# Kernel optimization log

Measured on AMD Instinct MI355X. Metric: run time of the kernel, lower is better.

## Reference

```python
import jax, jax.numpy as jnp
import numpy as np

# --- static config (mirrors init_kwargs) ---
T = 256          # number of tokens (decode steps)
A = 8            # analyses per token
N = 1 + T * A    # lattice rows (row 0 = start/gold row, token_idx 0)
H = 256          # encoder hidden size (bidirectional -> 2H context)
DH = 2 * H       # decoder hidden size (hidden_size * 2 per AnalysisDecoder)
FV, LV, TV, FEV = 100000, 50000, 100, 500   # vocab sizes
FD, LD, TD, FED = 300, 300, 100, 100        # embedding dims
D = FD + LD + TD + FED                      # 800 = LSTM input size
NEG = -1e10


def setup_inputs() -> dict:
    key = jax.random.key(0)
    ks = jax.random.split(key, 16)
    # structured lattice: [form, lemma, tag, feats x6, token_idx, is_gold]
    rng = np.random.default_rng(0)
    lat = np.zeros((N, 11), np.int64)
    lat[:, 0] = rng.integers(0, FV, N)
    lat[:, 1] = rng.integers(0, LV, N)
    lat[:, 2] = rng.integers(0, TV, N)
    lat[:, 3:9] = rng.integers(0, FEV, (N, 6))
    lat[:, 9] = np.concatenate([[0], np.repeat(np.arange(1, T + 1), A)])  # token_idx
    is_gold = np.zeros(N, np.int64)
    is_gold[0] = 1
    is_gold[1 + np.arange(T) * A] = 1   # exactly one gold analysis per token
    lat[:, 10] = is_gold

    s = 0.05
    def p(k, shape):
        return jax.random.normal(k, shape, dtype=jnp.float32) * s

    return dict(
        lattice=jnp.asarray(lat),
        num_tokens=T,
        form_emb=p(ks[0], (FV, FD)),
        lemma_emb=p(ks[1], (LV, LD)),
        tag_emb=p(ks[2], (TV, TD)),
        feats_emb=p(ks[3], (FEV, FED)),
        enc_wih_f=p(ks[4], (4 * H, D)), enc_whh_f=p(ks[5], (4 * H, H)), enc_b_f=p(ks[6], (4 * H,)),
        enc_wih_b=p(ks[7], (4 * H, D)), enc_whh_b=p(ks[8], (4 * H, H)), enc_b_b=p(ks[9], (4 * H,)),
        dec_wih=p(ks[10], (4 * DH, D)), dec_whh=p(ks[11], (4 * DH, DH)), dec_b=p(ks[12], (4 * DH,)),
    )


def _lstm_scan(xs, Wih, Whh, b, hdim):
    # batch-1 LSTM over a sequence; PyTorch gate order i, f, g, o
    def step(carry, x):
        h, c = carry
        g = Wih @ x + Whh @ h + b
        i, f, gg, o = jnp.split(g, 4)
        c = jax.nn.sigmoid(f) * c + jax.nn.sigmoid(i) * jnp.tanh(gg)
        h = jax.nn.sigmoid(o) * jnp.tanh(c)
        return (h, c), h
    z = jnp.zeros((hdim,), xs.dtype)
    (hT, cT), hs = jax.lax.scan(step, (z, z), xs)
    return hs, hT, cT


def reference(lattice, num_tokens, form_emb, lemma_emb, tag_emb, feats_emb,
              enc_wih_f, enc_whh_f, enc_b_f, enc_wih_b, enc_whh_b, enc_b_b,
              dec_wih, dec_whh, dec_b):
    tok = lattice[:, 9]
    gold = jnp.nonzero(lattice[:, 10], size=num_tokens + 1)[0]  # one gold per token (incl. start)

    # MorphEmbedding: concat of form/lemma/tag embeddings + mean of 6 feat embeddings
    emb = jnp.concatenate([
        form_emb[lattice[:, 0]],
        lemma_emb[lattice[:, 1]],
        tag_emb[lattice[:, 2]],
        feats_emb[lattice[:, 3:9]].mean(axis=1),
    ], axis=1)  # [N, D]

    # bidirectional encoder (dropouts are identity in eval)
    hs_f, hTf, cTf = _lstm_scan(emb, enc_wih_f, enc_whh_f, enc_b_f, H)
    hs_b, hTb, cTb = _lstm_scan(emb[::-1], enc_wih_b, enc_whh_b, enc_b_b, H)
    encoded = jnp.concatenate([hs_f, hs_b[::-1]], axis=1)  # [N, 2H]
    h0 = jnp.concatenate([hTf, hTb])  # decoder init hidden [DH]
    c0 = jnp.concatenate([cTf, cTb])

    # decode loop: NOTE the original never propagates the decoder hidden state
    # across steps (forward() discards the updated state) -- faithfully preserved.
    def dec(x, i):
        g = dec_wih @ x + dec_whh @ h0 + dec_b
        ii, ff, gg, oo = jnp.split(g, 4)
        c = jax.nn.sigmoid(ff) * c0 + jax.nn.sigmoid(ii) * jnp.tanh(gg)
        h = jax.nn.sigmoid(oo) * jnp.tanh(c)
        scores = encoded @ h                       # [N]
        scores = jnp.where(tok == i, scores, NEG)  # masked_fill(mask==0, -1e10)
        logp = jax.nn.log_softmax(scores)          # log_softmax over dim 0
        ptr = jnp.argmax(logp)
        return emb[ptr], (logp, ptr)               # greedy pointer feeds next step

    _, (pred_score, ptrs) = jax.lax.scan(dec, emb[0], jnp.arange(1, num_tokens + 1))
    pred_indices = jnp.concatenate([gold[:1], ptrs])

    # CrossEntropyLoss applied to log-probs (faithful: log_softmax applied again)
    lp = jax.nn.log_softmax(pred_score, axis=1)
    loss = -jnp.mean(lp[jnp.arange(num_tokens), gold[1:]])
    return pred_indices, loss
```

## Files before the change

kernel.cpp:

```cpp
#include <hip/hip_runtime.h>
#include <hip/hip_fp16.h>

#define T_TOK 256
#define NNODE 2049
#define HENC  256
#define DHID  512
#define DIN   800
#define G4    1024
#define DG4   2048

typedef _Float16 f16;
typedef _Float16 f16x2 __attribute__((ext_vector_type(2)));
typedef short    bf16x8 __attribute__((ext_vector_type(8)));
typedef float    f32x4  __attribute__((ext_vector_type(4)));

static __device__ __forceinline__ float sigm(float x){ return 1.0f/(1.0f+__expf(-x)); }
static __device__ __forceinline__ float tanhfast(float x){ return 1.0f - 2.0f/(__expf(2.0f*x)+1.0f); }

static __device__ __forceinline__ unsigned short f2bf(float x){
    unsigned u = __builtin_bit_cast(unsigned, x);
    unsigned r = (u + 0x7fffu + ((u>>16)&1u)) >> 16;
    return (unsigned short)r;
}
static __device__ __forceinline__ unsigned packh2(float a, float b){
    f16 ha = (f16)a, hb = (f16)b;
    unsigned short ua = __builtin_bit_cast(unsigned short, ha);
    unsigned short ub = __builtin_bit_cast(unsigned short, hb);
    return (unsigned)ua | ((unsigned)ub << 16);
}
static __device__ __forceinline__ float fdot2(unsigned wpk, unsigned hpk, float c){
#if __has_builtin(__builtin_amdgcn_fdot2)
    return __builtin_amdgcn_fdot2(__builtin_bit_cast(f16x2, wpk),
                                  __builtin_bit_cast(f16x2, hpk), c, false);
#else
    float d;
    asm volatile("v_dot2_f32_f16 %0, %1, %2, %3" : "=v"(d) : "v"(wpk), "v"(hpk), "v"(c));
    return d;
#endif
}

static __device__ __forceinline__ uint4 ldw_opaque(const uint4* p){
    uint4 r;
    asm volatile("global_load_dwordx4 %0, %1, off\n\ts_waitcnt vmcnt(0)"
                 : "=v"(r) : "v"(p));
    return r;
}

__global__ void k_embed(const int* __restrict__ lat,
                        const float* __restrict__ form, const float* __restrict__ lemma,
                        const float* __restrict__ tag,  const float* __restrict__ feats,
                        unsigned short* __restrict__ embB){
    int n = blockIdx.x;
    const int* L = lat + n*11;
    int i0 = L[0], i1 = L[1], i2 = L[2];
    for (int c = threadIdx.x; c < DIN; c += blockDim.x){
        float v;
        if (c < 300)      v = form[i0*300 + c];
        else if (c < 600) v = lemma[i1*300 + (c-300)];
        else if (c < 700) v = tag[i2*100 + (c-600)];
        else {
            float s = 0.f;
            #pragma unroll
            for (int j=0;j<6;++j) s += feats[L[3+j]*100 + (c-700)];
            v = s * (1.0f/6.0f);
        }
        embB[n*DIN + c] = f2bf(v);
    }
}

__global__ void k_f32_to_bf16(const float* __restrict__ src, unsigned short* __restrict__ dst, int n){
    int i = blockIdx.x*blockDim.x + threadIdx.x;
    if (i < n) dst[i] = f2bf(src[i]);
}

__global__ void k_pack_whh_v4(const float* __restrict__ wf, const float* __restrict__ wb,
                              uint4* __restrict__ wreg4){
    int id = blockIdx.x*blockDim.x + threadIdx.x;
    if (id >= 2048) return;
    int b = id >> 9, t = id & 511;
    int d = b >> 1, p = b & 1;
    const float* W = d ? wb : wf;
    int l = t & 63, w = t >> 6;
    int cq = l >> 4, j = w*16 + (l & 15);
    for (int g=0; g<4; ++g){
        const float* R = W + (size_t)(g*256 + p*128 + j)*256 + cq*64;
        for (int m=0; m<8; ++m){
            uint4 v;
            v.x = packh2(R[2*(m*4+0)], R[2*(m*4+0)+1]);
            v.y = packh2(R[2*(m*4+1)], R[2*(m*4+1)+1]);
            v.z = packh2(R[2*(m*4+2)], R[2*(m*4+2)+1]);
            v.w = packh2(R[2*(m*4+3)], R[2*(m*4+3)+1]);
            wreg4[((size_t)(b*32 + g*8 + m))*512 + t] = v;
        }
    }
}

__global__ __launch_bounds__(256) void k_gemm_bf16(const unsigned short* __restrict__ A,
                                                   const unsigned short* __restrict__ B,
                                                   float* __restrict__ C,
                                                   const float* __restrict__ bias,
                                                   int M, int Nc, int K){
    __shared__ unsigned short As[64][40];
    __shared__ unsigned short Bs[64][40];
    int m0 = blockIdx.x*64, n0 = blockIdx.y*64;
    int t = threadIdx.x, w = t>>6, lane = t&63;
    f32x4 acc[4];
    #pragma unroll
    for (int i=0;i<4;++i) acc[i] = (f32x4){0.f,0.f,0.f,0.f};
    int rowl = t>>2, kb0 = (t&3)*8;
    for (int k0=0; k0<K; k0+=32){
        uint4 av;
        int ar = m0 + rowl;
        if (ar < M) av = *(const uint4*)(A + (size_t)ar*K + k0 + kb0);
        else { av.x=av.y=av.z=av.w=0u; }
        *(uint4*)&As[rowl][kb0] = av;
        *(uint4*)&Bs[rowl][kb0] = *(const uint4*)(B + (size_t)(n0+rowl)*K + k0 + kb0);
        __syncthreads();
        int arow = w*16 + (lane&15), kk = (lane>>4)*8;
        bf16x8 af = *(const bf16x8*)&As[arow][kk];
        #pragma unroll
        for (int nt=0;nt<4;++nt){
            bf16x8 bf = *(const bf16x8*)&Bs[nt*16 + (lane&15)][kk];
            acc[nt] = __builtin_amdgcn_mfma_f32_16x16x32_bf16(af, bf, acc[nt], 0,0,0);
        }
        __syncthreads();
    }
    #pragma unroll
    for (int nt=0;nt<4;++nt){
        int col = n0 + nt*16 + (lane&15);
        float bb = bias ? bias[col] : 0.0f;
        #pragma unroll
        for (int r=0;r<4;++r){
            int row = m0 + w*16 + (lane>>4)*4 + r;
            if (row < M) C[(size_t)row*Nc + col] = acc[nt][r] + bb;
        }
    }
}

#define LOADW(g,m) const uint4 W##g##_##m = ldw_opaque(&wreg4[((size_t)(b*32 + g*8 + m))*512 + t]);

#define STEPM(m) { uint4 hv = sH4[cq*8 + m]; \
    a0 = fdot2(W0_##m.x, hv.x, a0); a0 = fdot2(W0_##m.y, hv.y, a0); \
    a0 = fdot2(W0_##m.z, hv.z, a0); a0 = fdot2(W0_##m.w, hv.w, a0); \
    a1 = fdot2(W1_##m.x, hv.x, a1); a1 = fdot2(W1_##m.y, hv.y, a1); \
    a1 = fdot2(W1_##m.z, hv.z, a1); a1 = fdot2(W1_##m.w, hv.w, a1); \
    a2 = fdot2(W2_##m.x, hv.x, a2); a2 = fdot2(W2_##m.y, hv.y, a2); \
    a2 = fdot2(W2_##m.z, hv.z, a2); a2 = fdot2(W2_##m.w, hv.w, a2); \
    a3 = fdot2(W3_##m.x, hv.x, a3); a3 = fdot2(W3_##m.y, hv.y, a3); \
    a3 = fdot2(W3_##m.z, hv.z, a3); a3 = fdot2(W3_##m.w, hv.w, a3); }

__global__ __launch_bounds__(512)
__attribute__((amdgpu_waves_per_eu(2,2)))
void k_lstm_scan(const uint4* __restrict__ wreg4,
                 const float* __restrict__ XgF,
                 const float* __restrict__ XgB,
                 int* __restrict__ flg,
                 float* __restrict__ xh,
                 float* __restrict__ encoded,
                 float* __restrict__ h0,
                 float* __restrict__ c0){
    __shared__ uint4 sH4[32];
    __shared__ float sG[512];
    int bid = blockIdx.x;
    int sub = bid >> 3, grp = bid & 7;
    if (grp >= 2) return;
    int d = grp, p = sub;
    int b  = d*2 + p;
    int pb = d*2 + (1-p);
    int t = threadIdx.x;
    int l = t & 63, w = t >> 6;
    int cq = l >> 4, j = w*16 + (l & 15);
    const float* Xg = d ? XgB : XgF;
    unsigned* sH32 = (unsigned*)sH4;
    f16* sHh = (f16*)sH4;

    LOADW(0,0) LOADW(0,1) LOADW(0,2) LOADW(0,3) LOADW(0,4) LOADW(0,5) LOADW(0,6) LOADW(0,7)
    LOADW(1,0) LOADW(1,1) LOADW(1,2) LOADW(1,3) LOADW(1,4) LOADW(1,5) LOADW(1,6) LOADW(1,7)
    LOADW(2,0) LOADW(2,1) LOADW(2,2) LOADW(2,3) LOADW(2,4) LOADW(2,5) LOADW(2,6) LOADW(2,7)
    LOADW(3,0) LOADW(3,1) LOADW(3,2) LOADW(3,3) LOADW(3,4) LOADW(3,5) LOADW(3,6) LOADW(3,7)

    if (t < 128) sH32[t] = 0u;
    float c_reg = 0.0f;
    __syncthreads();

    int node  = d ? (NNODE-1) : 0;
    int stepd = d ? -1 : 1;

    for (int s=0; s<NNODE; ++s){
        float xg0=0.f,xg1=0.f,xg2=0.f,xg3=0.f;
        if (cq == 0){
            const float* xr = Xg + (size_t)node*G4 + p*128 + j;
            xg0 = xr[0]; xg1 = xr[256]; xg2 = xr[512]; xg3 = xr[768];
        }
        float a0=0.f,a1=0.f,a2=0.f,a3=0.f;
        STEPM(0) STEPM(1) STEPM(2) STEPM(3) STEPM(4) STEPM(5) STEPM(6) STEPM(7)
        a0 += __shfl_xor(a0,16); a0 += __shfl_xor(a0,32);
        a1 += __shfl_xor(a1,16); a1 += __shfl_xor(a1,32);
        a2 += __shfl_xor(a2,16); a2 += __shfl_xor(a2,32);
        a3 += __shfl_xor(a3,16); a3 += __shfl_xor(a3,32);
        if (cq == 0){
            sG[0*128 + j] = a0 + xg0;
            sG[1*128 + j] = a1 + xg1;
            sG[2*128 + j] = a2 + xg2;
            sG[3*128 + j] = a3 + xg3;
        }
        __syncthreads();
        if (t < 128){
            float gi = sG[t], gf = sG[128+t], gg = sG[256+t], go = sG[384+t];
            float c = sigm(gf)*c_reg + sigm(gi)*tanhfast(gg);
            c_reg = c;
            float h = sigm(go)*tanhfast(c);
            __hip_atomic_store(&xh[((b*2) + (s&1))*128 + t], h,
                               __ATOMIC_RELAXED, __HIP_MEMORY_SCOPE_AGENT);
            sHh[p*128 + t] = (f16)h;
            encoded[(size_t)node*DHID + d*HENC + p*128 + t] = h;
            if (s == NNODE-1){ h0[d*HENC + p*128 + t] = h; c0[d*HENC + p*128 + t] = c; }
        }
        __syncthreads();
        if (t == 0){
            __hip_atomic_store(&flg[b], s+1, __ATOMIC_RELEASE, __HIP_MEMORY_SCOPE_AGENT);
            int iters = 0;
            while (__hip_atomic_load(&flg[pb], __ATOMIC_ACQUIRE, __HIP_MEMORY_SCOPE_AGENT) < s+1){
                if (++iters > (1<<26)) break;
            }
        }
        __syncthreads();
        if (t < 128){
            float hp = __hip_atomic_load(&xh[((pb*2) + (s&1))*128 + t],
                                         __ATOMIC_RELAXED, __HIP_MEMORY_SCOPE_AGENT);
            sHh[(1-p)*128 + t] = (f16)hp;
        }
        __syncthreads();
        node += stepd;
    }
}

__global__ void k_dec_const(const float* __restrict__ dec_whh, const float* __restrict__ dec_b,
                            const float* __restrict__ h0, float* __restrict__ Kd){
    __shared__ float sh[512];
    int t = threadIdx.x;
    int r = blockIdx.x*256 + t;
    sh[t] = h0[t]; sh[256+t] = h0[256+t];
    __syncthreads();
    float a = 0.f;
    const float* Wr = dec_whh + (size_t)r*512;
    for (int k=0;k<512;++k) a += Wr[k]*sh[k];
    Kd[r] = a + dec_b[r];
}

__global__ void k_hall(const float* __restrict__ G, const float* __restrict__ Kd,
                       const float* __restrict__ c0, float* __restrict__ Hall){
    int n = blockIdx.x, u = threadIdx.x;
    const float* g = G + (size_t)n*DG4;
    float gi = g[u]        + Kd[u];
    float gf = g[512+u]    + Kd[512+u];
    float gg = g[1024+u]   + Kd[1024+u];
    float go = g[1536+u]   + Kd[1536+u];
    float c  = sigm(gf)*c0[u] + sigm(gi)*tanhfast(gg);
    Hall[(size_t)n*DHID + u] = sigm(go)*tanhfast(c);
}

__global__ __launch_bounds__(256) void k_scores(const float* __restrict__ encoded,
                                                const float* __restrict__ Hall,
                                                float* __restrict__ S){
    __shared__ float sE[8][512];
    __shared__ float sHp[8][512];
    int i = blockIdx.x, t = threadIdx.x;
    for (int idx = t; idx < 8*512; idx += 256){
        int r = idx >> 9, c = idx & 511;
        int cand = 1 + i*8 + r;
        sE[r][c] = encoded[(size_t)cand*DHID + c];
        int prev = (i==0) ? 0 : (1 + (i-1)*8 + r);
        sHp[r][c] = Hall[(size_t)prev*DHID + c];
    }
    __syncthreads();
    int w = t>>6, lane = t&63;
    for (int q=0;q<16;++q){
        int pi = w*16 + q, p = pi>>3, c = pi&7;
        float v = 0.f;
        #pragma unroll
        for (int j=0;j<8;++j) v += sE[c][lane*8+j]*sHp[p][lane*8+j];
        #pragma unroll
        for (int off=32; off; off>>=1) v += __shfl_xor(v, off);
        if (lane==0) S[i*64 + p*8 + c] = v;
    }
}

__global__ __launch_bounds__(256) void k_decode(const float* __restrict__ S, float* __restrict__ out){
    __shared__ float nll[2048];
    __shared__ int   cst[2048];
    __shared__ int   path[256];
    __shared__ float wsum[4];
    int t = threadIdx.x;
    for (int p=0;p<8;++p){
        const float* s = S + t*64 + p*8;
        float m = s[0]; int am = 0;
        #pragma unroll
        for (int c=1;c<8;++c){ float v = s[c]; if (v > m){ m = v; am = c; } }
        float e = 0.f;
        #pragma unroll
        for (int c=0;c<8;++c) e += __expf(s[c]-m);
        float lse = m + __logf(e);
        nll[t*8+p] = lse - s[0];
        cst[t*8+p] = am;
    }
    __syncthreads();
    if (t == 0){
        int p = 0;
        for (int i=0;i<256;++i){
            int idx = i*8 + p;
            path[i] = idx;
            int c = cst[idx];
            out[i+1] = (float)(1 + i*8 + c);
            p = c;
        }
        out[0] = 0.0f;
    }
    __syncthreads();
    float v = nll[path[t]];
    #pragma unroll
    for (int off=32; off; off>>=1) v += __shfl_xor(v, off);
    if ((t&63)==0) wsum[t>>6] = v;
    __syncthreads();
    if (t==0) out[257] = (wsum[0]+wsum[1]+wsum[2]+wsum[3]) * (1.0f/256.0f);
}

extern "C" void kernel_launch(void* const* d_in, const int* in_sizes, int n_in,
                              void* d_out, int out_size, void* d_ws, size_t ws_size,
                              hipStream_t stream){
    (void)in_sizes; (void)n_in; (void)out_size; (void)ws_size;
    const int*   lattice  = (const int*)  d_in[0];
    const float* form     = (const float*)d_in[2];
    const float* lemma    = (const float*)d_in[3];
    const float* tag      = (const float*)d_in[4];
    const float* feats    = (const float*)d_in[5];
    const float* wih_f    = (const float*)d_in[6];
    const float* whh_f    = (const float*)d_in[7];
    const float* b_f      = (const float*)d_in[8];
    const float* wih_b    = (const float*)d_in[9];
    const float* whh_b    = (const float*)d_in[10];
    const float* b_b      = (const float*)d_in[11];
    const float* dwih     = (const float*)d_in[12];
    const float* dwhh     = (const float*)d_in[13];
    const float* db       = (const float*)d_in[14];
    float* out = (float*)d_out;

    char* ws = (char*)d_ws;
    size_t o = 0;
    auto alloc = [&](size_t bytes)->char*{ char* p = ws + o; o = (o + bytes + 255) & ~(size_t)255; return p; };
    int*            flg    = (int*)alloc(256);
    float*          xh     = (float*)alloc(4096);
    unsigned short* embB   = (unsigned short*)alloc((size_t)NNODE*DIN*2);
    unsigned short* wihfB  = (unsigned short*)alloc((size_t)G4*DIN*2);
    unsigned short* wihbB  = (unsigned short*)alloc((size_t)G4*DIN*2);
    unsigned short* dwihB  = (unsigned short*)alloc((size_t)DG4*DIN*2);
    uint4*          wreg4  = (uint4*)alloc((size_t)4*32*512*16);
    float*          XgF    = (float*)alloc((size_t)NNODE*G4*4);
    float*          XgB    = (float*)alloc((size_t)NNODE*G4*4);
    float*          Graw   = (float*)alloc((size_t)NNODE*DG4*4);
    float*          enc    = (float*)alloc((size_t)NNODE*DHID*4);
    float*          h0     = (float*)alloc(512*4);
    float*          c0     = (float*)alloc(512*4);
    float*          Kd     = (float*)alloc(2048*4);
    float*          Hall   = (float*)alloc((size_t)NNODE*DHID*4);
    float*          Sbuf   = (float*)alloc((size_t)256*64*4);

    hipMemsetAsync(d_ws, 0, 8192, stream);

    k_f32_to_bf16<<<(G4*DIN+255)/256, 256, 0, stream>>>(wih_f, wihfB, G4*DIN);
    k_f32_to_bf16<<<(G4*DIN+255)/256, 256, 0, stream>>>(wih_b, wihbB, G4*DIN);
    k_f32_to_bf16<<<(DG4*DIN+255)/256, 256, 0, stream>>>(dwih, dwihB, DG4*DIN);
    k_pack_whh_v4<<<8, 256, 0, stream>>>(whh_f, whh_b, wreg4);
    k_embed<<<NNODE, 256, 0, stream>>>(lattice, form, lemma, tag, feats, embB);

    dim3 gE((NNODE+63)/64, G4/64);
    k_gemm_bf16<<<gE, 256, 0, stream>>>(embB, wihfB, XgF, b_f, NNODE, G4, DIN);
    k_gemm_bf16<<<gE, 256, 0, stream>>>(embB, wihbB, XgB, b_b, NNODE, G4, DIN);
    dim3 gD((NNODE+63)/64, DG4/64);
    k_gemm_bf16<<<gD, 256, 0, stream>>>(embB, dwihB, Graw, nullptr, NNODE, DG4, DIN);

    k_lstm_scan<<<16, 512, 0, stream>>>(wreg4, XgF, XgB, flg, xh, enc, h0, c0);

    k_dec_const<<<8, 256, 0, stream>>>(dwhh, db, h0, Kd);
    k_hall<<<NNODE, 512, 0, stream>>>(Graw, Kd, c0, Hall);
    k_scores<<<256, 256, 0, stream>>>(enc, Hall, Sbuf);
    k_decode<<<1, 256, 0, stream>>>(Sbuf, out);
}
```

Baseline: 4.784 ms.

## Split each LSTM direction across four workgroups instead of two

The encoder recurrence now splits each direction's 256 hidden units across four 1024-thread workgroups of 64 units each, instead of two 512-thread workgroups of 128 units. Each thread holds a smaller slice of the recurrent weights in registers, which lowers register pressure and the per-thread dot-product length. The cost is a wider lane-shuffle reduction and a per-step barrier that waits on three peer flags instead of one. Each workgroup also reads the previous h from three peers through global memory, so cross-workgroup synchronisation latency may dominate.

```diff
diff --git a/kernel.cpp b/kernel.cpp
--- a/kernel.cpp
+++ b/kernel.cpp
@@ -73,24 +73,22 @@
     if (i < n) dst[i] = f2bf(src[i]);
 }
 
-__global__ void k_pack_whh_v4(const float* __restrict__ wf, const float* __restrict__ wb,
+__global__ void k_pack_whh_v5(const float* __restrict__ wf, const float* __restrict__ wb,
                               uint4* __restrict__ wreg4){
     int id = blockIdx.x*blockDim.x + threadIdx.x;
-    if (id >= 2048) return;
-    int b = id >> 9, t = id & 511;
-    int d = b >> 1, p = b & 1;
+    int b = id >> 10, t = id & 1023;
+    int d = b >> 2, p = b & 3;
     const float* W = d ? wb : wf;
-    int l = t & 63, w = t >> 6;
-    int cq = l >> 4, j = w*16 + (l & 15);
+    int u = t >> 4, cq = t & 15;
     for (int g=0; g<4; ++g){
-        const float* R = W + (size_t)(g*256 + p*128 + j)*256 + cq*64;
-        for (int m=0; m<8; ++m){
+        const float* R = W + (size_t)(g*256 + p*64 + u)*256 + cq*16;
+        for (int k=0; k<2; ++k){
             uint4 v;
-            v.x = packh2(R[2*(m*4+0)], R[2*(m*4+0)+1]);
-            v.y = packh2(R[2*(m*4+1)], R[2*(m*4+1)+1]);
-            v.z = packh2(R[2*(m*4+2)], R[2*(m*4+2)+1]);
-            v.w = packh2(R[2*(m*4+3)], R[2*(m*4+3)+1]);
-            wreg4[((size_t)(b*32 + g*8 + m))*512 + t] = v;
+            v.x = packh2(R[k*8+0], R[k*8+1]);
+            v.y = packh2(R[k*8+2], R[k*8+3]);
+            v.z = packh2(R[k*8+4], R[k*8+5]);
+            v.w = packh2(R[k*8+6], R[k*8+7]);
+            wreg4[((size_t)(b*8 + g*2 + k))*1024 + t] = v;
         }
     }
 }
@@ -137,20 +135,14 @@
     }
 }
 
-#define LOADW(g,m) const uint4 W##g##_##m = ldw_opaque(&wreg4[((size_t)(b*32 + g*8 + m))*512 + t]);
-
-#define STEPM(m) { uint4 hv = sH4[cq*8 + m]; \
-    a0 = fdot2(W0_##m.x, hv.x, a0); a0 = fdot2(W0_##m.y, hv.y, a0); \
-    a0 = fdot2(W0_##m.z, hv.z, a0); a0 = fdot2(W0_##m.w, hv.w, a0); \
-    a1 = fdot2(W1_##m.x, hv.x, a1); a1 = fdot2(W1_##m.y, hv.y, a1); \
-    a1 = fdot2(W1_##m.z, hv.z, a1); a1 = fdot2(W1_##m.w, hv.w, a1); \
-    a2 = fdot2(W2_##m.x, hv.x, a2); a2 = fdot2(W2_##m.y, hv.y, a2); \
-    a2 = fdot2(W2_##m.z, hv.z, a2); a2 = fdot2(W2_##m.w, hv.w, a2); \
-    a3 = fdot2(W3_##m.x, hv.x, a3); a3 = fdot2(W3_##m.y, hv.y, a3); \
-    a3 = fdot2(W3_##m.z, hv.z, a3); a3 = fdot2(W3_##m.w, hv.w, a3); }
-
-__global__ __launch_bounds__(512)
-__attribute__((amdgpu_waves_per_eu(2,2)))
+#define LOADW(g,k) const uint4 W##g##_##k = ldw_opaque(&wreg4[((size_t)(b*8 + g*2 + k))*1024 + t]);
+
+#define G8(A, P, Q) A = fdot2(P.x,hv0.x,A); A = fdot2(P.y,hv0.y,A); \
+                    A = fdot2(P.z,hv0.z,A); A = fdot2(P.w,hv0.w,A); \
+                    A = fdot2(Q.x,hv1.x,A); A = fdot2(Q.y,hv1.y,A); \
+                    A = fdot2(Q.z,hv1.z,A); A = fdot2(Q.w,hv1.w,A);
+
+__global__ __launch_bounds__(1024)
 void k_lstm_scan(const uint4* __restrict__ wreg4,
                  const float* __restrict__ XgF,
                  const float* __restrict__ XgB,
@@ -160,24 +152,19 @@
                  float* __restrict__ h0,
                  float* __restrict__ c0){
     __shared__ uint4 sH4[32];
-    __shared__ float sG[512];
+    __shared__ float sG[256];
     int bid = blockIdx.x;
-    int sub = bid >> 3, grp = bid & 7;
-    if (grp >= 2) return;
-    int d = grp, p = sub;
-    int b  = d*2 + p;
-    int pb = d*2 + (1-p);
+    int d = bid & 7, p = bid >> 3;
+    if (d >= 2) return;
+    int b = d*4 + p;
     int t = threadIdx.x;
-    int l = t & 63, w = t >> 6;
-    int cq = l >> 4, j = w*16 + (l & 15);
+    int u = t >> 4, cq = t & 15;
     const float* Xg = d ? XgB : XgF;
     unsigned* sH32 = (unsigned*)sH4;
     f16* sHh = (f16*)sH4;
 
-    LOADW(0,0) LOADW(0,1) LOADW(0,2) LOADW(0,3) LOADW(0,4) LOADW(0,5) LOADW(0,6) LOADW(0,7)
-    LOADW(1,0) LOADW(1,1) LOADW(1,2) LOADW(1,3) LOADW(1,4) LOADW(1,5) LOADW(1,6) LOADW(1,7)
-    LOADW(2,0) LOADW(2,1) LOADW(2,2) LOADW(2,3) LOADW(2,4) LOADW(2,5) LOADW(2,6) LOADW(2,7)
-    LOADW(3,0) LOADW(3,1) LOADW(3,2) LOADW(3,3) LOADW(3,4) LOADW(3,5) LOADW(3,6) LOADW(3,7)
+    LOADW(0,0) LOADW(0,1) LOADW(1,0) LOADW(1,1)
+    LOADW(2,0) LOADW(2,1) LOADW(3,0) LOADW(3,1)
 
     if (t < 128) sH32[t] = 0u;
     float c_reg = 0.0f;
@@ -187,48 +174,64 @@
     int stepd = d ? -1 : 1;
 
     for (int s=0; s<NNODE; ++s){
-        float xg0=0.f,xg1=0.f,xg2=0.f,xg3=0.f;
+        float xi=0.f, xf=0.f, xgg=0.f, xo=0.f;
+        if (t < 64){
+            const float* xr = Xg + (size_t)node*G4 + p*64 + t;
+            xi  = xr[0];
+            xf  = xr[256];
+            xgg = xr[512];
+            xo  = xr[768];
+        }
+        uint4 hv0 = sH4[cq*2];
+        uint4 hv1 = sH4[cq*2+1];
+        float a0=0.f,a1=0.f,a2=0.f,a3=0.f;
+        G8(a0, W0_0, W0_1)
+        G8(a1, W1_0, W1_1)
+        G8(a2, W2_0, W2_1)
+        G8(a3, W3_0, W3_1)
+        a0 += __shfl_xor(a0,1); a0 += __shfl_xor(a0,2); a0 += __shfl_xor(a0,4); a0 += __shfl_xor(a0,8);
+        a1 += __shfl_xor(a1,1); a1 += __shfl_xor(a1,2); a1 += __shfl_xor(a1,4); a1 += __shfl_xor(a1,8);
+        a2 += __shfl_xor(a2,1); a2 += __shfl_xor(a2,2); a2 += __shfl_xor(a2,4); a2 += __shfl_xor(a2,8);
+        a3 += __shfl_xor(a3,1); a3 += __shfl_xor(a3,2); a3 += __shfl_xor(a3,4); a3 += __shfl_xor(a3,8);
         if (cq == 0){
-            const float* xr = Xg + (size_t)node*G4 + p*128 + j;
-            xg0 = xr[0]; xg1 = xr[256]; xg2 = xr[512]; xg3 = xr[768];
-        }
-        float a0=0.f,a1=0.f,a2=0.f,a3=0.f;
-        STEPM(0) STEPM(1) STEPM(2) STEPM(3) STEPM(4) STEPM(5) STEPM(6) STEPM(7)
-        a0 += __shfl_xor(a0,16); a0 += __shfl_xor(a0,32);
-        a1 += __shfl_xor(a1,16); a1 += __shfl_xor(a1,32);
-        a2 += __shfl_xor(a2,16); a2 += __shfl_xor(a2,32);
-        a3 += __shfl_xor(a3,16); a3 += __shfl_xor(a3,32);
-        if (cq == 0){
-            sG[0*128 + j] = a0 + xg0;
-            sG[1*128 + j] = a1 + xg1;
-            sG[2*128 + j] = a2 + xg2;
-            sG[3*128 + j] = a3 + xg3;
-        }
-        __syncthreads();
-        if (t < 128){
-            float gi = sG[t], gf = sG[128+t], gg = sG[256+t], go = sG[384+t];
+            sG[u]       = a0;
+            sG[64 + u]  = a1;
+            sG[128 + u] = a2;
+            sG[192 + u] = a3;
+        }
+        __syncthreads();
+        if (t < 64){
+            float gi = sG[t] + xi, gf = sG[64+t] + xf;
+            float gg = sG[128+t] + xgg, go = sG[192+t] + xo;
             float c = sigm(gf)*c_reg + sigm(gi)*tanhfast(gg);
             c_reg = c;
             float h = sigm(go)*tanhfast(c);
-            __hip_atomic_store(&xh[((b*2) + (s&1))*128 + t], h,
+            __hip_atomic_store(&xh[((b*2) + (s&1))*64 + t], h,
                                __ATOMIC_RELAXED, __HIP_MEMORY_SCOPE_AGENT);
-            sHh[p*128 + t] = (f16)h;
-            encoded[(size_t)node*DHID + d*HENC + p*128 + t] = h;
-            if (s == NNODE-1){ h0[d*HENC + p*128 + t] = h; c0[d*HENC + p*128 + t] = c; }
+            sHh[p*64 + t] = (f16)h;
+            encoded[(size_t)node*DHID + d*HENC + p*64 + t] = h;
+            if (s == NNODE-1){ h0[d*HENC + p*64 + t] = h; c0[d*HENC + p*64 + t] = c; }
         }
         __syncthreads();
         if (t == 0){
             __hip_atomic_store(&flg[b], s+1, __ATOMIC_RELEASE, __HIP_MEMORY_SCOPE_AGENT);
-            int iters = 0;
-            while (__hip_atomic_load(&flg[pb], __ATOMIC_ACQUIRE, __HIP_MEMORY_SCOPE_AGENT) < s+1){
-                if (++iters > (1<<26)) break;
+            int base = d*4;
+            long iters = 0;
+            #pragma unroll
+            for (int q=0;q<4;++q){
+                if (q == p) continue;
+                while (__hip_atomic_load(&flg[base+q], __ATOMIC_ACQUIRE, __HIP_MEMORY_SCOPE_AGENT) < s+1){
+                    if (++iters > (1L<<27)) break;
+                }
             }
         }
         __syncthreads();
-        if (t < 128){
-            float hp = __hip_atomic_load(&xh[((pb*2) + (s&1))*128 + t],
+        if (t < 192){
+            int qq = t >> 6;
+            int q = qq + (qq >= p ? 1 : 0);
+            float hp = __hip_atomic_load(&xh[((d*4+q)*2 + (s&1))*64 + (t&63)],
                                          __ATOMIC_RELAXED, __HIP_MEMORY_SCOPE_AGENT);
-            sHh[(1-p)*128 + t] = (f16)hp;
+            sHh[q*64 + (t&63)] = (f16)hp;
         }
         __syncthreads();
         node += stepd;
@@ -354,7 +357,7 @@
     unsigned short* wihfB  = (unsigned short*)alloc((size_t)G4*DIN*2);
     unsigned short* wihbB  = (unsigned short*)alloc((size_t)G4*DIN*2);
     unsigned short* dwihB  = (unsigned short*)alloc((size_t)DG4*DIN*2);
-    uint4*          wreg4  = (uint4*)alloc((size_t)4*32*512*16);
+    uint4*          wreg4  = (uint4*)alloc((size_t)8*8*1024*16);
     float*          XgF    = (float*)alloc((size_t)NNODE*G4*4);
     float*          XgB    = (float*)alloc((size_t)NNODE*G4*4);
     float*          Graw   = (float*)alloc((size_t)NNODE*DG4*4);
@@ -370,7 +373,7 @@
     k_f32_to_bf16<<<(G4*DIN+255)/256, 256, 0, stream>>>(wih_f, wihfB, G4*DIN);
     k_f32_to_bf16<<<(G4*DIN+255)/256, 256, 0, stream>>>(wih_b, wihbB, G4*DIN);
     k_f32_to_bf16<<<(DG4*DIN+255)/256, 256, 0, stream>>>(dwih, dwihB, DG4*DIN);
-    k_pack_whh_v4<<<8, 256, 0, stream>>>(whh_f, whh_b, wreg4);
+    k_pack_whh_v5<<<8, 1024, 0, stream>>>(whh_f, whh_b, wreg4);
     k_embed<<<NNODE, 256, 0, stream>>>(lattice, form, lemma, tag, feats, embB);
 
     dim3 gE((NNODE+63)/64, G4/64);
@@ -379,7 +382,7 @@
     dim3 gD((NNODE+63)/64, DG4/64);
     k_gemm_bf16<<<gD, 256, 0, stream>>>(embB, dwihB, Graw, nullptr, NNODE, DG4, DIN);
 
-    k_lstm_scan<<<16, 512, 0, stream>>>(wreg4, XgF, XgB, flg, xh, enc, h0, c0);
+    k_lstm_scan<<<32, 1024, 0, stream>>>(wreg4, XgF, XgB, flg, xh, enc, h0, c0);
 
     k_dec_const<<<8, 256, 0, stream>>>(dwhh, db, h0, Kd);
     k_hall<<<NNODE, 512, 0, stream>>>(Graw, Kd, c0, Hall);
```

New measurement: 6.779 ms. 1.42x slower.
